# Kernel optimization log

Measured on AMD Instinct MI355X. Metric: run time of the kernel, lower is better.

The kernel has to match this reference:

```python
import jax, jax.numpy as jnp
import numpy as np

B, S, D, H = 4, 2048, 1024, 16
DK = D // H
THETA = 10000.0


def _rope(x, pos):
    # x: [..., S, DK]; interleaved-pair rotation as in the torch module
    dk = x.shape[-1]
    inv_freq = 1.0 / (THETA ** (jnp.arange(0, dk, 2, dtype=jnp.float32) / dk))  # [dk/2]
    freqs = pos.astype(jnp.float32)[:, None] * inv_freq  # [S, dk/2]
    cos, sin = jnp.cos(freqs), jnp.sin(freqs)
    xr = x.reshape(*x.shape[:-1], dk // 2, 2)
    x0, x1 = xr[..., 0], xr[..., 1]
    rot = jnp.stack([x0 * cos - x1 * sin, x0 * sin + x1 * cos], axis=-1)
    return rot.reshape(x.shape)


def setup_inputs() -> dict:
    key = jax.random.key(0)
    ks = jax.random.split(key, 5)
    scale = 0.02
    return {
        "x": jax.random.normal(ks[0], (B, S, D), dtype=jnp.float32),
        "Wq": jax.random.normal(ks[1], (D, D), dtype=jnp.float32) * scale,
        "Wk": jax.random.normal(ks[2], (D, D), dtype=jnp.float32) * scale,
        "Wv": jax.random.normal(ks[3], (D, D), dtype=jnp.float32) * scale,
        "Wo": jax.random.normal(ks[4], (D, D), dtype=jnp.float32) * scale,
    }


def reference(x, Wq, Wk, Wv, Wo):
    b, s, d = x.shape
    pos = jnp.arange(s)
    # projections (Linear with no bias, y = x @ W^T)
    q = jnp.einsum('bsd,ed->bse', x, Wq).reshape(b, s, H, DK).transpose(0, 2, 1, 3)
    k = jnp.einsum('bsd,ed->bse', x, Wk).reshape(b, s, H, DK).transpose(0, 2, 1, 3)
    v = jnp.einsum('bsd,ed->bse', x, Wv).reshape(b, s, H, DK).transpose(0, 2, 1, 3)
    q = _rope(q, pos)
    k = _rope(k, pos)
    scores = jnp.einsum('bhqd,bhkd->bhqk', q, k) / jnp.sqrt(jnp.float32(DK))
    causal = jnp.tril(jnp.ones((s, s), dtype=bool))
    scores = jnp.where(causal, scores, -jnp.inf)
    attn = jax.nn.softmax(scores, axis=-1)
    out = jnp.einsum('bhqk,bhkd->bhqd', attn, v)
    out = out.transpose(0, 2, 1, 3).reshape(b, s, d)
    return jnp.einsum('bsd,ed->bse', out, Wo)
```

## Files before the change

kernel.cpp:

```cpp
#include <hip/hip_runtime.h>

#define B_  4
#define S_  2048
#define D_  1024
#define H_  16
#define DK_ 64
#define BH_ (B_*H_)
#define L2E 1.44269504088896f

typedef __attribute__((ext_vector_type(8))) short bf16x8;
typedef __attribute__((ext_vector_type(4))) float f32x4;
typedef __attribute__((ext_vector_type(16))) float f32x16;
typedef __attribute__((ext_vector_type(4))) unsigned u32x4;
typedef unsigned short u16;

__device__ __forceinline__ u16 f2bf(float f){
  unsigned u = __builtin_bit_cast(unsigned, f);
  u += 0x7fffu + ((u >> 16) & 1u);
  return (u16)(u >> 16);
}
__device__ __forceinline__ float bf2f(u16 h){
  unsigned u = ((unsigned)h) << 16;
  return __builtin_bit_cast(float, u);
}

#define GLD16(g,l) __builtin_amdgcn_global_load_lds( \
    (const __attribute__((address_space(1))) void*)(g), \
    (__attribute__((address_space(3))) void*)(l), 16, 0, 0)

#define MFMA16(a,b,c) __builtin_amdgcn_mfma_f32_16x16x32_bf16((a),(b),(c),0,0,0)
#define MFMA32(a,b,c) __builtin_amdgcn_mfma_f32_32x32x16_bf16((a),(b),(c),0,0,0)

__global__ void cast_kernel(const float4* __restrict__ in, ushort4* __restrict__ out, int n4){
  int i = blockIdx.x*blockDim.x + threadIdx.x;
  int stride = gridDim.x*blockDim.x;
  for (; i < n4; i += stride){
    float4 v = in[i];
    ushort4 o;
    o.x = f2bf(v.x); o.y = f2bf(v.y); o.z = f2bf(v.z); o.w = f2bf(v.w);
    out[i] = o;
  }
}

__global__ void cast4_kernel(const float4* __restrict__ w0, const float4* __restrict__ w1,
                             const float4* __restrict__ w2, const float4* __restrict__ w3,
                             ushort4* __restrict__ out){
  const int per = D_*D_/4;
  int i = blockIdx.x*blockDim.x + threadIdx.x;
  int stride = gridDim.x*blockDim.x;
  for (; i < 4*per; i += stride){
    int m = i / per, r = i - m*per;
    const float4* src = (m==0)?w0:(m==1)?w1:(m==2)?w2:w3;
    float4 v = src[r];
    ushort4 o;
    o.x = f2bf(v.x); o.y = f2bf(v.y); o.z = f2bf(v.z); o.w = f2bf(v.w);
    out[i] = o;
  }
}

__global__ void trig_kernel(float* __restrict__ ct, float* __restrict__ st){
  int t = blockIdx.x*blockDim.x + threadIdx.x;
  int i = t & 31, s = t >> 5;
  float expo = -(float)(2*i) * (1.0f/(float)DK_);
  float inv = powf(10000.0f, expo);
  float ang = (float)s * inv;
  ct[t] = cosf(ang);
  st[t] = sinf(ang);
}

template<int MODE>
__global__ __launch_bounds__(256, 2)
void gemm_bt(const u16* __restrict__ A,
             const u16* __restrict__ B0, const u16* __restrict__ B1, const u16* __restrict__ B2,
             u16* __restrict__ O0, u16* __restrict__ O1, u16* __restrict__ O2,
             float* __restrict__ Cf,
             const float* __restrict__ ct, const float* __restrict__ st, int K){
  __shared__ __align__(16) u16 lAB[2*128*64];
  u16* const lA = lAB;
  u16* const lB = lAB + 128*64;

  const int id = (int)blockIdx.x;
  const int nchunk = (MODE==0) ? 192 : 64;
  const int swz = (id & 7)*nchunk + (id >> 3);
  int z = 0, rem = swz;
  if (MODE == 0){ z = swz >> 9; rem = swz & 511; }
  const int m0 = (rem >> 3) * 128, n0 = (rem & 7) * 128;

  const u16* Bm = B0;
  u16* Om = O0;
  if (MODE == 0){
    if (z == 1){ Bm = B1; Om = O1; }
    else if (z == 2){ Bm = B2; Om = O2; }
  }
  const int tid = threadIdx.x, wave = tid>>6, lane = tid&63;
  const int wm = wave>>1, wn = wave&1;
  const int srow = lane>>3, scol = (lane&7)*8;

  f32x4 acc[4][4];
  #pragma unroll
  for (int m=0;m<4;++m)
    #pragma unroll
    for (int n=0;n<4;++n) acc[m][n] = (f32x4){0.f,0.f,0.f,0.f};

  #pragma unroll 1
  for (int k0 = 0; k0 < K; k0 += 64){
    #pragma unroll
    for (int j=0;j<4;++j){
      int rb = (wave*4 + j)*8;
      GLD16(A  + (size_t)(m0 + rb + srow)*K + k0 + scol, lA + rb*64);
      GLD16(Bm + (size_t)(n0 + rb + srow)*K + k0 + scol, lB + rb*64);
    }
    __syncthreads();
    #pragma unroll
    for (int kk=0;kk<2;++kk){
      bf16x8 af[4], bfr[4];
      #pragma unroll
      for (int m=0;m<4;++m) af[m]  = *(const bf16x8*)&lA[(wm*64 + m*16 + (lane&15))*64 + kk*32 + (lane>>4)*8];
      #pragma unroll
      for (int n=0;n<4;++n) bfr[n] = *(const bf16x8*)&lB[(wn*64 + n*16 + (lane&15))*64 + kk*32 + (lane>>4)*8];
      #pragma unroll
      for (int m=0;m<4;++m)
        #pragma unroll
        for (int n=0;n<4;++n)
          acc[m][n] = MFMA16(af[m], bfr[n], acc[m][n]);
    }
    __syncthreads();
  }

  if (MODE == 0 && z != 2){
    const float scale = (z == 0) ? 0.125f : 1.0f;
    #pragma unroll
    for (int m=0;m<4;++m){
      const int lr0 = wm*64 + m*16 + ((lane>>4)<<2);
      #pragma unroll
      for (int n=0;n<4;++n){
        const int lc = wn*64 + n*16 + (lane&15);
        #pragma unroll
        for (int r=0;r<4;++r){
          const int lr = lr0 + r;
          lAB[lr*128 + (lc ^ (((lr>>2)&7)<<4))] = f2bf(acc[m][n][r]);
        }
      }
    }
    __syncthreads();
    #pragma unroll
    for (int k=0;k<8;++k){
      const int cid = k*256 + tid;
      const int rr = cid >> 4, cc = cid & 15;
      bf16x8 v = *(const bf16x8*)&lAB[rr*128 + ((cc*8) ^ (((rr>>2)&7)<<4))];
      const int i = m0 + rr, bb = i >> 11, s = i & (S_-1);
      const int e0 = n0 + cc*8, h = e0 >> 6, dk0 = e0 & 63;
      const float4 c4 = *(const float4*)(ct + s*32 + (dk0>>1));
      const float4 s4 = *(const float4*)(st + s*32 + (dk0>>1));
      const float cc4[4] = {c4.x,c4.y,c4.z,c4.w};
      const float ss4[4] = {s4.x,s4.y,s4.z,s4.w};
      bf16x8 o;
      #pragma unroll
      for (int j=0;j<4;++j){
        const float x0 = bf2f((u16)v[2*j]);
        const float x1 = bf2f((u16)v[2*j+1]);
        o[2*j]   = (short)f2bf((x0*cc4[j] - x1*ss4[j])*scale);
        o[2*j+1] = (short)f2bf((x0*ss4[j] + x1*cc4[j])*scale);
      }
      *(bf16x8*)(Om + ((size_t)((bb*H_ + h)*S_ + s))*DK_ + dk0) = o;
    }
  } else {
    #pragma unroll
    for (int m=0;m<4;++m){
      const int rb = m0 + wm*64 + m*16 + ((lane>>4)<<2);
      #pragma unroll
      for (int n=0;n<4;++n){
        const int e = n0 + wn*64 + n*16 + (lane&15);
        if (MODE == 0){
          const int h = e>>6, dk = e&63;
          const int b = rb >> 11, s0 = rb & (S_-1);
          ushort4 w4;
          w4.x = f2bf(acc[m][n][0]); w4.y = f2bf(acc[m][n][1]);
          w4.z = f2bf(acc[m][n][2]); w4.w = f2bf(acc[m][n][3]);
          *(ushort4*)(Om + ((size_t)((b*H_ + h)*DK_ + dk))*S_ + s0) = w4;
        } else {
          #pragma unroll
          for (int r=0;r<4;++r)
            Cf[(size_t)(rb + r)*D_ + e] = acc[m][n][r];
        }
      }
    }
  }
}

__global__ __launch_bounds__(256, 4)
void attn_kernel(const u16* __restrict__ Q, const u16* __restrict__ K,
                 const u16* __restrict__ Vt, u16* __restrict__ O){
  __shared__ __align__(16) u16 lK[2][64*64];
  __shared__ __align__(16) u16 lV[2][64*64];

  const int bh = blockIdx.x;
  const int qmap[16] = {15,14,13,12, 10,11,9,8, 5,4,6,7, 0,1,2,3};
  const int qt = qmap[blockIdx.y];
  const int b = bh >> 4, h = bh & 15;
  const int tid = threadIdx.x, wave = tid>>6, lane = tid&63;
  const int hi = lane >> 5, l31 = lane & 31;
  const int qw = qt*128 + wave*32;
  const int qg = qw + l31;
  const u16* Qb = Q  + (size_t)bh*S_*DK_;
  const u16* Kb = K  + (size_t)bh*S_*DK_;
  const u16* Vb = Vt + (size_t)bh*DK_*S_;

  bf16x8 qf[4];
  #pragma unroll
  for (int ds=0; ds<4; ++ds)
    qf[ds] = *(const bf16x8*)(Qb + (size_t)qg*DK_ + ds*16 + hi*8);

  f32x16 oacc[2];
  oacc[0] = (f32x16)0.f; oacc[1] = (f32x16)0.f;
  float m_run = -1e30f, l_run = 0.f;

  const int srow8 = lane >> 3;
  const int csw = ((lane&7) ^ srow8) << 3;

  const int kv_end = (qt+1)*128;

  #pragma unroll
  for (int it=0; it<2; ++it){
    const int rb = (it*4 + wave)*8;
    const int row = rb + srow8;
    GLD16(Kb + (size_t)row*DK_ + csw, lK[0] + rb*64);
    GLD16(Vb + (size_t)row*S_ + csw,  lV[0] + rb*64);
  }
  __syncthreads();

  int cur = 0;
  for (int kv0 = 0; kv0 < kv_end; kv0 += 64){
    const int nxt = kv0 + 64;
    if (nxt < kv_end){
      #pragma unroll
      for (int it=0; it<2; ++it){
        const int rb = (it*4 + wave)*8;
        const int row = rb + srow8;
        GLD16(Kb + (size_t)(nxt+row)*DK_ + csw, lK[cur^1] + rb*64);
        GLD16(Vb + (size_t)row*S_ + nxt + csw,  lV[cur^1] + rb*64);
      }
    }

    if (kv0 < qw + 32){
      f32x16 sacc[2];
      sacc[0] = (f32x16)0.f; sacc[1] = (f32x16)0.f;
      __builtin_amdgcn_s_setprio(1);
      #pragma unroll
      for (int kb=0; kb<2; ++kb){
        const int krow = kb*32 + l31;
        #pragma unroll
        for (int ds=0; ds<4; ++ds){
          bf16x8 kf = *(const bf16x8*)&lK[cur][krow*64 + (((ds*2+hi) ^ (krow&7))<<3)];
          sacc[kb] = MFMA32(kf, qf[ds], sacc[kb]);
        }
      }
      __builtin_amdgcn_s_setprio(0);

      if (kv0 + 63 > qw){
        #pragma unroll
        for (int kb=0; kb<2; ++kb)
          #pragma unroll
          for (int r=0; r<16; ++r){
            const int kvg = kv0 + kb*32 + 4*hi + (r&3) + 8*(r>>2);
            if (kvg > qg) sacc[kb][r] = -1e30f;
          }
      }

      float mx = sacc[0][0];
      #pragma unroll
      for (int r=1; r<16; ++r) mx = fmaxf(mx, sacc[0][r]);
      #pragma unroll
      for (int r=0; r<16; ++r) mx = fmaxf(mx, sacc[1][r]);
      mx = fmaxf(mx, __shfl_xor(mx, 32));
      if (!__all((mx - m_run)*L2E <= 8.0f)){
        const float mn = fmaxf(m_run, mx);
        const float alpha = exp2f((m_run - mn)*L2E);
        m_run = mn;
        l_run *= alpha;
        oacc[0] *= alpha;
        oacc[1] *= alpha;
      }
      const float nc = m_run * L2E;
      float ps = 0.f;
      #pragma unroll
      for (int kb=0; kb<2; ++kb)
        #pragma unroll
        for (int r=0; r<16; ++r){
          float v = exp2f(__builtin_fmaf(sacc[kb][r], L2E, -nc));
          sacc[kb][r] = v;
          ps += v;
        }
      ps += __shfl_xor(ps, 32);
      l_run += ps;

      bf16x8 pa[4];
      #pragma unroll
      for (int kb=0; kb<2; ++kb){
        unsigned w[8];
        #pragma unroll
        for (int i=0; i<8; ++i){
          float a = sacc[kb][2*i], b2 = sacc[kb][2*i+1];
          asm("v_cvt_pk_bf16_f32 %0, %1, %2" : "=v"(w[i]) : "v"(a), "v"(b2));
        }
        auto s02 = __builtin_amdgcn_permlane32_swap(w[0], w[2], false, false);
        auto s13 = __builtin_amdgcn_permlane32_swap(w[1], w[3], false, false);
        auto s46 = __builtin_amdgcn_permlane32_swap(w[4], w[6], false, false);
        auto s57 = __builtin_amdgcn_permlane32_swap(w[5], w[7], false, false);
        u32x4 ua = {s02[0], s13[0], s02[1], s13[1]};
        u32x4 ub = {s46[0], s57[0], s46[1], s57[1]};
        pa[kb*2+0] = __builtin_bit_cast(bf16x8, ua);
        pa[kb*2+1] = __builtin_bit_cast(bf16x8, ub);
      }

      __builtin_amdgcn_s_setprio(1);
      #pragma unroll
      for (int dkb=0; dkb<2; ++dkb){
        const int vrow = dkb*32 + l31;
        #pragma unroll
        for (int ks=0; ks<4; ++ks){
          bf16x8 vf = *(const bf16x8*)&lV[cur][vrow*64 + (((ks*2+hi) ^ (vrow&7))<<3)];
          oacc[dkb] = MFMA32(vf, pa[ks], oacc[dkb]);
        }
      }
      __builtin_amdgcn_s_setprio(0);
    }
    __syncthreads();
    cur ^= 1;
  }

  const float inv = 1.0f / l_run;
  #pragma unroll
  for (int dkb=0; dkb<2; ++dkb)
    #pragma unroll
    for (int rq=0; rq<4; ++rq){
      ushort4 w4;
      w4.x = f2bf(oacc[dkb][rq*4+0]*inv);
      w4.y = f2bf(oacc[dkb][rq*4+1]*inv);
      w4.z = f2bf(oacc[dkb][rq*4+2]*inv);
      w4.w = f2bf(oacc[dkb][rq*4+3]*inv);
      const int dk0 = dkb*32 + 8*rq + 4*hi;
      *(ushort4*)(O + (size_t)(b*S_+qg)*D_ + h*DK_ + dk0) = w4;
    }
}

extern "C" void kernel_launch(void* const* d_in, const int* in_sizes, int n_in,
                              void* d_out, int out_size, void* d_ws, size_t ws_size,
                              hipStream_t stream){
  const float* x  = (const float*)d_in[0];
  const float* Wq = (const float*)d_in[1];
  const float* Wk = (const float*)d_in[2];
  const float* Wv = (const float*)d_in[3];
  const float* Wo = (const float*)d_in[4];
  float* out = (float*)d_out;
  char* ws = (char*)d_ws;

  size_t off = 0;
  u16* xb  = (u16*)(ws + off); off += (size_t)B_*S_*D_*2;
  u16* wqb = (u16*)(ws + off); off += (size_t)D_*D_*2;
  u16* wkb = (u16*)(ws + off); off += (size_t)D_*D_*2;
  u16* wvb = (u16*)(ws + off); off += (size_t)D_*D_*2;
  u16* wob = (u16*)(ws + off); off += (size_t)D_*D_*2;
  u16* Qb  = (u16*)(ws + off); off += (size_t)BH_*S_*DK_*2;
  u16* Kb  = (u16*)(ws + off); off += (size_t)BH_*S_*DK_*2;
  u16* Vtb = (u16*)(ws + off); off += (size_t)BH_*S_*DK_*2;
  u16* Ob  = (u16*)(ws + off); off += (size_t)B_*S_*D_*2;
  float* ct = (float*)(ws + off); off += (size_t)S_*32*4;
  float* st = (float*)(ws + off); off += (size_t)S_*32*4;

  cast_kernel<<<2048,256,0,stream>>>((const float4*)x,  (ushort4*)xb,  B_*S_*D_/4);
  cast4_kernel<<<1024,256,0,stream>>>((const float4*)Wq, (const float4*)Wk,
                                      (const float4*)Wv, (const float4*)Wo, (ushort4*)wqb);
  trig_kernel<<<(S_*32)/256,256,0,stream>>>(ct, st);

  gemm_bt<0><<<1536,256,0,stream>>>(xb, wqb,wkb,wvb, Qb,Kb,Vtb, nullptr, ct, st, D_);

  attn_kernel<<<dim3(BH_, S_/128),256,0,stream>>>(Qb, Kb, Vtb, Ob);

  gemm_bt<1><<<512,256,0,stream>>>(Ob, wob,wob,wob, nullptr,nullptr,nullptr, out, nullptr, nullptr, D_);
}
```

Baseline: 177.6 us.

## Split long causal attention tiles across two KV halves and fuse prep kernels

The upper eight query tiles of each head are now split into two blocks, each covering half of the key/value range. Each half writes unnormalized bf16 partial outputs plus its running max and sum, and a new merge kernel rescales and combines the two halves. This is meant to even out causal-mask imbalance across blocks and shorten the critical path, at the cost of one extra launch, extra partial-output traffic, and bf16 rounding of the partials. Separately, the x cast, weight cast and trig-table kernels are folded into one launch to cut launch overhead, and the partial buffers reuse workspace regions that are dead by then.

```diff
diff --git a/kernel.cpp b/kernel.cpp
--- a/kernel.cpp
+++ b/kernel.cpp
@@ -31,41 +31,41 @@
 #define MFMA16(a,b,c) __builtin_amdgcn_mfma_f32_16x16x32_bf16((a),(b),(c),0,0,0)
 #define MFMA32(a,b,c) __builtin_amdgcn_mfma_f32_32x32x16_bf16((a),(b),(c),0,0,0)
 
-__global__ void cast_kernel(const float4* __restrict__ in, ushort4* __restrict__ out, int n4){
-  int i = blockIdx.x*blockDim.x + threadIdx.x;
-  int stride = gridDim.x*blockDim.x;
-  for (; i < n4; i += stride){
-    float4 v = in[i];
-    ushort4 o;
-    o.x = f2bf(v.x); o.y = f2bf(v.y); o.z = f2bf(v.z); o.w = f2bf(v.w);
-    out[i] = o;
-  }
-}
-
-__global__ void cast4_kernel(const float4* __restrict__ w0, const float4* __restrict__ w1,
-                             const float4* __restrict__ w2, const float4* __restrict__ w3,
-                             ushort4* __restrict__ out){
-  const int per = D_*D_/4;
-  int i = blockIdx.x*blockDim.x + threadIdx.x;
-  int stride = gridDim.x*blockDim.x;
-  for (; i < 4*per; i += stride){
-    int m = i / per, r = i - m*per;
-    const float4* src = (m==0)?w0:(m==1)?w1:(m==2)?w2:w3;
-    float4 v = src[r];
-    ushort4 o;
-    o.x = f2bf(v.x); o.y = f2bf(v.y); o.z = f2bf(v.z); o.w = f2bf(v.w);
-    out[i] = o;
-  }
-}
-
-__global__ void trig_kernel(float* __restrict__ ct, float* __restrict__ st){
-  int t = blockIdx.x*blockDim.x + threadIdx.x;
-  int i = t & 31, s = t >> 5;
-  float expo = -(float)(2*i) * (1.0f/(float)DK_);
-  float inv = powf(10000.0f, expo);
-  float ang = (float)s * inv;
-  ct[t] = cosf(ang);
-  st[t] = sinf(ang);
+__global__ void prep_kernel(const float4* __restrict__ x,
+                            const float4* __restrict__ w0, const float4* __restrict__ w1,
+                            const float4* __restrict__ w2, const float4* __restrict__ w3,
+                            ushort4* __restrict__ xb, ushort4* __restrict__ wb,
+                            float* __restrict__ ct, float* __restrict__ st){
+  const int bid = blockIdx.x;
+  if (bid < 2048){
+    const int n4 = B_*S_*D_/4;
+    int i = bid*blockDim.x + threadIdx.x;
+    for (; i < n4; i += 2048*256){
+      float4 v = x[i];
+      ushort4 o;
+      o.x = f2bf(v.x); o.y = f2bf(v.y); o.z = f2bf(v.z); o.w = f2bf(v.w);
+      xb[i] = o;
+    }
+  } else if (bid < 3072){
+    const int per = D_*D_/4;
+    int i = (bid-2048)*blockDim.x + threadIdx.x;
+    for (; i < 4*per; i += 1024*256){
+      int m = i / per, r = i - m*per;
+      const float4* src = (m==0)?w0:(m==1)?w1:(m==2)?w2:w3;
+      float4 v = src[r];
+      ushort4 o;
+      o.x = f2bf(v.x); o.y = f2bf(v.y); o.z = f2bf(v.z); o.w = f2bf(v.w);
+      wb[i] = o;
+    }
+  } else {
+    const int t = (bid-3072)*blockDim.x + threadIdx.x;
+    const int i = t & 31, s = t >> 5;
+    float expo = -(float)(2*i) * (1.0f/(float)DK_);
+    float inv = powf(10000.0f, expo);
+    float ang = (float)s * inv;
+    ct[t] = cosf(ang);
+    st[t] = sinf(ang);
+  }
 }
 
 template<int MODE>
@@ -190,13 +190,16 @@
 
 __global__ __launch_bounds__(256, 4)
 void attn_kernel(const u16* __restrict__ Q, const u16* __restrict__ K,
-                 const u16* __restrict__ Vt, u16* __restrict__ O){
+                 const u16* __restrict__ Vt, u16* __restrict__ O,
+                 u16* __restrict__ Opart, float* __restrict__ Mlb){
   __shared__ __align__(16) u16 lK[2][64*64];
   __shared__ __align__(16) u16 lV[2][64*64];
 
   const int bh = blockIdx.x;
-  const int qmap[16] = {15,14,13,12, 10,11,9,8, 5,4,6,7, 0,1,2,3};
-  const int qt = qmap[blockIdx.y];
+  const int qtv[24] = {15,15,7,14,14,13,13,6,12,12,5,11,11,4,10,10,3,9,9,2,8,8,1,0};
+  const int hfv[24] = {0,1,-1,0,1,0,1,-1,0,1,-1,0,1,-1,0,1,-1,0,1,-1,0,1,-1,-1};
+  const int qt = qtv[blockIdx.y];
+  const int hf = hfv[blockIdx.y];
   const int b = bh >> 4, h = bh & 15;
   const int tid = threadIdx.x, wave = tid>>6, lane = tid&63;
   const int hi = lane >> 5, l31 = lane & 31;
@@ -206,6 +209,9 @@
   const u16* Kb = K  + (size_t)bh*S_*DK_;
   const u16* Vb = Vt + (size_t)bh*DK_*S_;
 
+  const int kv_begin = (hf == 1) ? (qt+1)*64 : 0;
+  const int kv_end   = (hf == 0) ? (qt+1)*64 : (qt+1)*128;
+
   bf16x8 qf[4];
   #pragma unroll
   for (int ds=0; ds<4; ++ds)
@@ -218,19 +224,17 @@
   const int srow8 = lane >> 3;
   const int csw = ((lane&7) ^ srow8) << 3;
 
-  const int kv_end = (qt+1)*128;
-
   #pragma unroll
   for (int it=0; it<2; ++it){
     const int rb = (it*4 + wave)*8;
     const int row = rb + srow8;
-    GLD16(Kb + (size_t)row*DK_ + csw, lK[0] + rb*64);
-    GLD16(Vb + (size_t)row*S_ + csw,  lV[0] + rb*64);
+    GLD16(Kb + (size_t)(kv_begin+row)*DK_ + csw, lK[0] + rb*64);
+    GLD16(Vb + (size_t)row*S_ + kv_begin + csw,  lV[0] + rb*64);
   }
   __syncthreads();
 
   int cur = 0;
-  for (int kv0 = 0; kv0 < kv_end; kv0 += 64){
+  for (int kv0 = kv_begin; kv0 < kv_end; kv0 += 64){
     const int nxt = kv0 + 64;
     if (nxt < kv_end){
       #pragma unroll
@@ -329,19 +333,71 @@
     cur ^= 1;
   }
 
-  const float inv = 1.0f / l_run;
+  if (hf < 0){
+    const float inv = 1.0f / l_run;
+    #pragma unroll
+    for (int dkb=0; dkb<2; ++dkb)
+      #pragma unroll
+      for (int rq=0; rq<4; ++rq){
+        ushort4 w4;
+        w4.x = f2bf(oacc[dkb][rq*4+0]*inv);
+        w4.y = f2bf(oacc[dkb][rq*4+1]*inv);
+        w4.z = f2bf(oacc[dkb][rq*4+2]*inv);
+        w4.w = f2bf(oacc[dkb][rq*4+3]*inv);
+        const int dk0 = dkb*32 + 8*rq + 4*hi;
+        *(ushort4*)(O + (size_t)(b*S_+qg)*D_ + h*DK_ + dk0) = w4;
+      }
+  } else {
+    const size_t pidx = (size_t)((bh*8 + (qt-8))*2 + hf);
+    u16* Pp = Opart + pidx*8192;
+    float* Mp = Mlb + pidx*256;
+    const int ql = wave*32 + l31;
+    #pragma unroll
+    for (int dkb=0; dkb<2; ++dkb)
+      #pragma unroll
+      for (int rq=0; rq<4; ++rq){
+        ushort4 w4;
+        w4.x = f2bf(oacc[dkb][rq*4+0]);
+        w4.y = f2bf(oacc[dkb][rq*4+1]);
+        w4.z = f2bf(oacc[dkb][rq*4+2]);
+        w4.w = f2bf(oacc[dkb][rq*4+3]);
+        const int dk0 = dkb*32 + 8*rq + 4*hi;
+        *(ushort4*)(Pp + ql*64 + dk0) = w4;
+      }
+    if (hi == 0){ Mp[ql*2] = m_run; Mp[ql*2+1] = l_run; }
+  }
+}
+
+__global__ void merge_kernel(const u16* __restrict__ Opart,
+                             const float* __restrict__ Mlb,
+                             u16* __restrict__ O){
+  const int bx = blockIdx.x;
+  const int bh = bx >> 3, qh = bx & 7;
+  const int b = bh >> 4, h = bh & 15;
+  const int qt = qh + 8;
+  const size_t base = (size_t)((bh*8 + qh)*2);
+  const u16* P0 = Opart + base*8192;
+  const u16* P1 = P0 + 8192;
+  const float* M0 = Mlb + base*256;
+  const float* M1 = M0 + 256;
   #pragma unroll
-  for (int dkb=0; dkb<2; ++dkb)
-    #pragma unroll
-    for (int rq=0; rq<4; ++rq){
-      ushort4 w4;
-      w4.x = f2bf(oacc[dkb][rq*4+0]*inv);
-      w4.y = f2bf(oacc[dkb][rq*4+1]*inv);
-      w4.z = f2bf(oacc[dkb][rq*4+2]*inv);
-      w4.w = f2bf(oacc[dkb][rq*4+3]*inv);
-      const int dk0 = dkb*32 + 8*rq + 4*hi;
-      *(ushort4*)(O + (size_t)(b*S_+qg)*D_ + h*DK_ + dk0) = w4;
-    }
+  for (int k=0;k<4;++k){
+    const int c = k*256 + threadIdx.x;
+    const int q = c >> 3, ck = c & 7;
+    const float m0 = M0[q*2], l0 = M0[q*2+1];
+    const float m1 = M1[q*2], l1 = M1[q*2+1];
+    const float ms = fmaxf(m0, m1);
+    const float a0 = exp2f((m0 - ms)*L2E);
+    const float a1 = exp2f((m1 - ms)*L2E);
+    const float inv = 1.0f / (l0*a0 + l1*a1);
+    bf16x8 v0 = *(const bf16x8*)&P0[q*64 + ck*8];
+    bf16x8 v1 = *(const bf16x8*)&P1[q*64 + ck*8];
+    bf16x8 o;
+    #pragma unroll
+    for (int j=0;j<8;++j)
+      o[j] = (short)f2bf((bf2f((u16)v0[j])*a0 + bf2f((u16)v1[j])*a1)*inv);
+    *(bf16x8*)(O + ((size_t)(b*S_ + qt*128 + q))*D_ + h*DK_ + ck*8) = o;
+  }
 }
 
 extern "C" void kernel_launch(void* const* d_in, const int* in_sizes, int n_in,
@@ -368,14 +424,19 @@
   float* ct = (float*)(ws + off); off += (size_t)S_*32*4;
   float* st = (float*)(ws + off); off += (size_t)S_*32*4;
 
-  cast_kernel<<<2048,256,0,stream>>>((const float4*)x,  (ushort4*)xb,  B_*S_*D_/4);
-  cast4_kernel<<<1024,256,0,stream>>>((const float4*)Wq, (const float4*)Wk,
-                                      (const float4*)Wv, (const float4*)Wo, (ushort4*)wqb);
-  trig_kernel<<<(S_*32)/256,256,0,stream>>>(ct, st);
+  u16* Opart = xb;
+  float* Mlb = (float*)wqb;
+
+  prep_kernel<<<3328,256,0,stream>>>((const float4*)x,
+                                     (const float4*)Wq, (const float4*)Wk,
+                                     (const float4*)Wv, (const float4*)Wo,
+                                     (ushort4*)xb, (ushort4*)wqb, ct, st);
 
   gemm_bt<0><<<1536,256,0,stream>>>(xb, wqb,wkb,wvb, Qb,Kb,Vtb, nullptr, ct, st, D_);
 
-  attn_kernel<<<dim3(BH_, S_/128),256,0,stream>>>(Qb, Kb, Vtb, Ob);
+  attn_kernel<<<dim3(BH_, 24),256,0,stream>>>(Qb, Kb, Vtb, Ob, Opart, Mlb);
+
+  merge_kernel<<<512,256,0,stream>>>(Opart, Mlb, Ob);
 
   gemm_bt<1><<<512,256,0,stream>>>(Ob, wob,wob,wob, nullptr,nullptr,nullptr, out, nullptr, nullptr, D_);
 }
```

New measurement: 189.8 us. 6.9% more time.
